# Performance work log

Measured on AMD Instinct MI355X. Metric: run time of the kernel, lower is better.

## Reference

```python
import jax, jax.numpy as jnp
import numpy as np

N_HEAD = 16
HEAD_DIM = 64
WINDOW = 256
ROPE_BASE = 10000.0


def _rope_cos_sin(seq_len, dtype):
    inv_freq = 1.0 / (ROPE_BASE ** (jnp.arange(0, HEAD_DIM, 2, dtype=jnp.float32) / HEAD_DIM))
    t = jnp.arange(seq_len, dtype=jnp.float32)
    freqs = jnp.outer(t, inv_freq)                      # [S, D/2]
    emb = jnp.concatenate([freqs, freqs], axis=-1)      # [S, D]
    return jnp.cos(emb).astype(dtype), jnp.sin(emb).astype(dtype)


def _rotate_half(x):
    x1, x2 = jnp.split(x, 2, axis=-1)
    return jnp.concatenate([-x2, x1], axis=-1)


def _apply_rope(x, cos, sin):
    # x: [B, H, S, D]; cos/sin: [S, D]
    return x * cos[None, None, :, :] + _rotate_half(x) * sin[None, None, :, :]


def setup_inputs() -> dict:
    key = jax.random.key(0)
    ks = jax.random.split(key, 5)
    B, S, E = 2, 2048, 1024
    scale = 1.0 / np.sqrt(E)
    return {
        "x": jax.random.normal(ks[0], (B, S, E), dtype=jnp.float32),
        "Wq": jax.random.normal(ks[1], (E, E), dtype=jnp.float32) * scale,
        "Wk": jax.random.normal(ks[2], (E, E), dtype=jnp.float32) * scale,
        "Wv": jax.random.normal(ks[3], (E, E), dtype=jnp.float32) * scale,
        "Wo": jax.random.normal(ks[4], (E, E), dtype=jnp.float32) * scale,
    }


def reference(x, Wq, Wk, Wv, Wo):
    B, S, E = x.shape
    # QKV projections (nn.Linear: x @ W.T), split heads -> [B, H, S, D]
    def proj(W):
        return (x @ W.T).reshape(B, S, N_HEAD, HEAD_DIM).transpose(0, 2, 1, 3)
    q, k, v = proj(Wq), proj(Wk), proj(Wv)

    cos, sin = _rope_cos_sin(S, x.dtype)
    q = _apply_rope(q, cos, sin)
    k = _apply_rope(k, cos, sin)

    # banded causal mask: attend iff 0 <= i - j < WINDOW
    pos = jnp.arange(S)
    rel = pos[:, None] - pos[None, :]
    allowed = (rel >= 0) & (rel < WINDOW)                # [S, S]

    scale = 1.0 / np.sqrt(HEAD_DIM)
    att = jnp.einsum("bhqd,bhkd->bhqk", q, k) * scale    # [B, H, S, S]
    att = jnp.where(allowed[None, None, :, :], att, -jnp.inf)
    att = jax.nn.softmax(att.astype(jnp.float32), axis=-1).astype(x.dtype)
    y = jnp.einsum("bhqk,bhkd->bhqd", att, v)
    y = y.transpose(0, 2, 1, 3).reshape(B, S, E)
    return y @ Wo.T
```

## Files before the change

kernel.cpp:

```cpp
#include <hip/hip_runtime.h>
#include <cstdint>
#include <cstddef>

#define AS1 __attribute__((address_space(1)))
#define AS3 __attribute__((address_space(3)))

typedef __attribute__((ext_vector_type(4))) float f32x4;
typedef __attribute__((ext_vector_type(2))) float f32x2;
typedef __attribute__((ext_vector_type(8))) short bf16x8;
typedef unsigned short u16;
typedef unsigned int u32;

#define B_ 2
#define S_ 2048
#define E_ 1024
#define H_ 16
#define D_ 64
#define M_ 4096

__device__ __forceinline__ u16 f2bf(float f) {
  union { float f; u32 u; } v; v.f = f;
  u32 u = v.u;
  u32 r = (u + 0x7FFFu + ((u >> 16) & 1u)) >> 16;
  return (u16)r;
}
__device__ __forceinline__ float bf2f(u16 h) {
  union { u32 u; float f; } v; v.u = ((u32)h) << 16;
  return v.f;
}

__device__ __forceinline__ void gl2lds16(const void* g, void* l) {
  __builtin_amdgcn_global_load_lds((const AS1 void*)g, (AS3 void*)l, 16, 0, 0);
}

__global__ __launch_bounds__(256) void prep_kernel(
    const float* __restrict__ x, const float* __restrict__ wq,
    const float* __restrict__ wk, const float* __restrict__ wv,
    const float* __restrict__ wo,
    u16* __restrict__ xb, u16* __restrict__ wqkv, u16* __restrict__ wob,
    float* __restrict__ cstab)
{
  int idx = blockIdx.x * 256 + threadIdx.x;
  const int NX4 = (M_ * E_) / 4;
  const int NW4 = (E_ * E_) / 4;
  const int CONV_TOTAL = NX4 + 4 * NW4;
  if (idx < CONV_TOTAL) {
    const float* src; u16* dst; int off;
    if (idx < NX4)                { src = x;  dst = xb;              off = idx; }
    else if (idx < NX4 + NW4)     { src = wq; dst = wqkv;            off = idx - NX4; }
    else if (idx < NX4 + 2 * NW4) { src = wk; dst = wqkv + E_ * E_;  off = idx - NX4 - NW4; }
    else if (idx < NX4 + 3 * NW4) { src = wv; dst = wqkv + 2 * E_ * E_; off = idx - NX4 - 2 * NW4; }
    else                          { src = wo; dst = wob;             off = idx - NX4 - 3 * NW4; }
    float4 v = reinterpret_cast<const float4*>(src)[off];
    ushort4 o;
    o.x = f2bf(v.x); o.y = f2bf(v.y); o.z = f2bf(v.z); o.w = f2bf(v.w);
    reinterpret_cast<ushort4*>(dst)[off] = o;
  } else if (idx < CONV_TOTAL + S_ * 32) {
    int e = idx - CONV_TOTAL;
    int s = e >> 5, i = e & 31;
    double invf = pow(10000.0, -(double)i / 32.0);
    double ang = (double)s * invf;
    cstab[e * 2]     = (float)cos(ang);
    cstab[e * 2 + 1] = (float)sin(ang);
  }
}

template <int MODE>
__global__ __launch_bounds__(256) void gemm_bt(
    const u16* __restrict__ A, const u16* __restrict__ Bm,
    u16* __restrict__ q_out, u16* __restrict__ k_out, u16* __restrict__ vt_out,
    float* __restrict__ f_out, const float* __restrict__ cstab)
{
  __shared__ __align__(16) u16 smem[17408];
  u16* lA = smem;
  u16* lB = smem + 8192;
  const int tid = threadIdx.x;
  const int w = tid >> 6, l = tid & 63;
  const int lr = l & 15, lg = l >> 4;
  const int mt = blockIdx.y, nt = blockIdx.x;
  const int woffm = (w >> 1) * 64, woffn = (w & 1) * 64;

  const int srow = l >> 3;
  const int scol = ((l & 7) ^ srow) * 8;
  const u16* Abase = A + (size_t)(mt * 128) * 1024;
  const u16* Bbase = Bm + (size_t)(nt * 128) * 1024;

  f32x4 acc[4][4];
#pragma unroll
  for (int i = 0; i < 4; ++i)
#pragma unroll
    for (int j = 0; j < 4; ++j) acc[i][j] = (f32x4){0.f, 0.f, 0.f, 0.f};

  for (int kt = 0; kt < 1024; kt += 64) {
    __syncthreads();
#pragma unroll
    for (int i = 0; i < 4; ++i) {
      int ch = w * 4 + i;
      int row = ch * 8 + srow;
      gl2lds16(Abase + row * 1024 + kt + scol, &lA[ch * 512]);
      gl2lds16(Bbase + row * 1024 + kt + scol, &lB[ch * 512]);
    }
    __syncthreads();
#pragma unroll
    for (int kk = 0; kk < 2; ++kk) {
      bf16x8 av[4], bv[4];
#pragma unroll
      for (int mf = 0; mf < 4; ++mf) {
        int row = woffm + mf * 16 + lr;
        int byteoff = row * 128 + ((kk * 64 + lg * 16) ^ ((row & 7) << 4));
        av[mf] = *(const bf16x8*)((const char*)lA + byteoff);
      }
#pragma unroll
      for (int nf = 0; nf < 4; ++nf) {
        int row = woffn + nf * 16 + lr;
        int byteoff = row * 128 + ((kk * 64 + lg * 16) ^ ((row & 7) << 4));
        bv[nf] = *(const bf16x8*)((const char*)lB + byteoff);
      }
#pragma unroll
      for (int mf = 0; mf < 4; ++mf)
#pragma unroll
        for (int nf = 0; nf < 4; ++nf)
          acc[mf][nf] = __builtin_amdgcn_mfma_f32_16x16x32_bf16(
              av[mf], bv[nf], acc[mf][nf], 0, 0, 0);
    }
  }

  __syncthreads();

  if (MODE == 0) {
    int n0 = nt * 128 + woffn;
    int wsel = n0 >> 10;
    int hh = (n0 >> 6) & 15;
    int stile = mt * 128 + woffm;
    int b = stile >> 11;
    int s0 = stile & 2047;
    if (wsel == 2) {
#pragma unroll
      for (int mf = 0; mf < 4; ++mf) {
        int s = s0 + mf * 16 + lg * 4;
#pragma unroll
        for (int nf = 0; nf < 4; ++nf) {
          int d = nf * 16 + lr;
          ushort4 pk;
          pk.x = f2bf(acc[mf][nf][0]); pk.y = f2bf(acc[mf][nf][1]);
          pk.z = f2bf(acc[mf][nf][2]); pk.w = f2bf(acc[mf][nf][3]);
          *reinterpret_cast<ushort4*>(
              vt_out + ((size_t)(b * 16 + hh) * 64 + d) * 2048 + s) = pk;
        }
      }
    } else {
      u16* lt = smem + w * (64 * 68);
      const f32x2* cst = (const f32x2*)cstab;
#pragma unroll
      for (int mf = 0; mf < 4; ++mf) {
        int sl = mf * 16 + lg * 4;
#pragma unroll
        for (int rr = 0; rr < 4; ++rr) {
          int s = s0 + sl + rr;
#pragma unroll
          for (int nf = 0; nf < 2; ++nf) {
            int i = nf * 16 + lr;
            f32x2 cs = cst[s * 32 + i];
            float a = acc[mf][nf][rr], bb = acc[mf][nf + 2][rr];
            lt[(sl + rr) * 68 + i]      = f2bf(a * cs.x - bb * cs.y);
            lt[(sl + rr) * 68 + 32 + i] = f2bf(bb * cs.x + a * cs.y);
          }
        }
      }
      asm volatile("s_waitcnt lgkmcnt(0)" ::: "memory");
      u16* gout = (wsel == 0 ? q_out : k_out) +
                  ((size_t)(b * 16 + hh) * 2048 + s0) * 64;
      int rl = l >> 3, cc = l & 7;
#pragma unroll
      for (int it = 0; it < 8; ++it) {
        int row = it * 8 + rl;
        bf16x8 v = *(const bf16x8*)(lt + row * 68 + cc * 8);
        *(bf16x8*)(gout + (size_t)row * 64 + cc * 8) = v;
      }
    }
  } else {
#pragma unroll
    for (int mf = 0; mf < 4; ++mf) {
      int m = mt * 128 + woffm + mf * 16 + lg * 4;
#pragma unroll
      for (int nf = 0; nf < 4; ++nf) {
        int n = nt * 128 + woffn + nf * 16 + lr;
#pragma unroll
        for (int rr = 0; rr < 4; ++rr)
          f_out[(size_t)(m + rr) * 1024 + n] = acc[mf][nf][rr];
      }
    }
  }
}

__global__ __launch_bounds__(256) void attn_kernel(
    const u16* __restrict__ qb, const u16* __restrict__ kb,
    const u16* __restrict__ vt, u16* __restrict__ yb)
{
  int blk = blockIdx.x;
  int qt = blk & 31, h = (blk >> 5) & 15, b = blk >> 9;
  int w = threadIdx.x >> 6, l = threadIdx.x & 63;
  int lr = l & 15, lg = l >> 4;
  int qbase = qt * 64 + w * 16;

  const u16* Q  = qb + ((size_t)(b * 16 + h) * 2048) * 64;
  const u16* Kp = kb + ((size_t)(b * 16 + h) * 2048) * 64;
  const u16* Vp = vt + ((size_t)(b * 16 + h) * 64) * 2048;

  __shared__ __align__(16) u16 lds_p[4][16 * 40];
  u16* myp = &lds_p[w][0];

  bf16x8 aq0 = *(const bf16x8*)(Q + (size_t)(qbase + lr) * 64 + lg * 8);
  bf16x8 aq1 = *(const bf16x8*)(Q + (size_t)(qbase + lr) * 64 + 32 + lg * 8);

  f32x4 o[4];
#pragma unroll
  for (int i = 0; i < 4; ++i) o[i] = (f32x4){0.f, 0.f, 0.f, 0.f};
  float mrun[4], lsum[4];
#pragma unroll
  for (int r = 0; r < 4; ++r) { mrun[r] = -1e30f; lsum[r] = 0.f; }

  int kstart = qbase - 255; if (kstart < 0) kstart = 0;
  kstart &= ~31;
  int kend = qbase + 16;
  const float scale = 0.125f;

  for (int kt = kstart; kt < kend; kt += 32) {
    bf16x8 bk0a = *(const bf16x8*)(Kp + (size_t)(kt + lr) * 64 + lg * 8);
    bf16x8 bk0b = *(const bf16x8*)(Kp + (size_t)(kt + lr) * 64 + 32 + lg * 8);
    bf16x8 bk1a = *(const bf16x8*)(Kp + (size_t)(kt + 16 + lr) * 64 + lg * 8);
    bf16x8 bk1b = *(const bf16x8*)(Kp + (size_t)(kt + 16 + lr) * 64 + 32 + lg * 8);
    f32x4 s0 = (f32x4){0.f, 0.f, 0.f, 0.f};
    f32x4 s1 = (f32x4){0.f, 0.f, 0.f, 0.f};
    s0 = __builtin_amdgcn_mfma_f32_16x16x32_bf16(aq0, bk0a, s0, 0, 0, 0);
    s0 = __builtin_amdgcn_mfma_f32_16x16x32_bf16(aq1, bk0b, s0, 0, 0, 0);
    s1 = __builtin_amdgcn_mfma_f32_16x16x32_bf16(aq0, bk1a, s1, 0, 0, 0);
    s1 = __builtin_amdgcn_mfma_f32_16x16x32_bf16(aq1, bk1b, s1, 0, 0, 0);

    float p0[4], p1[4];
#pragma unroll
    for (int r = 0; r < 4; ++r) {
      int q = qbase + lg * 4 + r;
      int k0 = kt + lr, k1 = k0 + 16;
      int r0 = q - k0, r1 = q - k1;
      float v0 = (r0 >= 0 && r0 < 256) ? s0[r] * scale : -1e30f;
      float v1 = (r1 >= 0 && r1 < 256) ? s1[r] * scale : -1e30f;
      float pmax = fmaxf(v0, v1);
      if (!__all(pmax <= mrun[r] + 8.0f)) {
        float mx = pmax;
        mx = fmaxf(mx, __shfl_xor(mx, 1));
        mx = fmaxf(mx, __shfl_xor(mx, 2));
        mx = fmaxf(mx, __shfl_xor(mx, 4));
        mx = fmaxf(mx, __shfl_xor(mx, 8));
        float mnew = fmaxf(mrun[r], mx);
        float f = __expf(mrun[r] - mnew);
        mrun[r] = mnew;
        lsum[r] *= f;
#pragma unroll
        for (int nf = 0; nf < 4; ++nf) o[nf][r] *= f;
      }
      p0[r] = __expf(v0 - mrun[r]);
      p1[r] = __expf(v1 - mrun[r]);
      lsum[r] += p0[r] + p1[r];
    }

#pragma unroll
    for (int r = 0; r < 4; ++r) {
      myp[(lg * 4 + r) * 40 + lr]      = f2bf(p0[r]);
      myp[(lg * 4 + r) * 40 + 16 + lr] = f2bf(p1[r]);
    }
    asm volatile("s_waitcnt lgkmcnt(0)" ::: "memory");
    bf16x8 pa = *(const bf16x8*)((const char*)myp + lr * 80 + lg * 16);
    asm volatile("s_waitcnt lgkmcnt(0)" ::: "memory");

#pragma unroll
    for (int df = 0; df < 4; ++df) {
      bf16x8 vv = *(const bf16x8*)(Vp + (size_t)(df * 16 + lr) * 2048 + kt + lg * 8);
      o[df] = __builtin_amdgcn_mfma_f32_16x16x32_bf16(pa, vv, o[df], 0, 0, 0);
    }
  }

  float lrun[4];
#pragma unroll
  for (int r = 0; r < 4; ++r) {
    float sm = lsum[r];
    sm += __shfl_xor(sm, 1);
    sm += __shfl_xor(sm, 2);
    sm += __shfl_xor(sm, 4);
    sm += __shfl_xor(sm, 8);
    lrun[r] = 1.f / sm;
  }
#pragma unroll
  for (int df = 0; df < 4; ++df)
#pragma unroll
    for (int r = 0; r < 4; ++r) {
      int s = qbase + lg * 4 + r;
      int d = df * 16 + lr;
      yb[((size_t)(b * 2048 + s)) * 1024 + h * 64 + d] = f2bf(o[df][r] * lrun[r]);
    }
}

extern "C" void kernel_launch(void* const* d_in, const int* in_sizes, int n_in,
                              void* d_out, int out_size, void* d_ws, size_t ws_size,
                              hipStream_t stream) {
  const float* x  = (const float*)d_in[0];
  const float* wq = (const float*)d_in[1];
  const float* wk = (const float*)d_in[2];
  const float* wv = (const float*)d_in[3];
  const float* wo = (const float*)d_in[4];

  char* ws = (char*)d_ws;
  const size_t MB = 1u << 20;
  if (ws_size < 49 * MB) return;
  u16*   xb   = (u16*)(ws);
  u16*   wqkv = (u16*)(ws + 8 * MB);
  u16*   wob  = (u16*)(ws + 14 * MB);
  u16*   qb   = (u16*)(ws + 16 * MB);
  u16*   kb   = (u16*)(ws + 24 * MB);
  u16*   vt   = (u16*)(ws + 32 * MB);
  u16*   yb   = (u16*)(ws + 40 * MB);
  float* cst  = (float*)(ws + 48 * MB);
  float* out  = (float*)d_out;

  prep_kernel<<<8448, 256, 0, stream>>>(x, wq, wk, wv, wo, xb, wqkv, wob, cst);
  gemm_bt<0><<<dim3(24, 32), 256, 0, stream>>>(xb, wqkv, qb, kb, vt, nullptr, cst);
  attn_kernel<<<1024, 256, 0, stream>>>(qb, kb, vt, yb);
  gemm_bt<1><<<dim3(8, 32), 256, 0, stream>>>(yb, wob, nullptr, nullptr, nullptr, out, nullptr);
}
```

Before: 190.1 us.

## Rewrite QKV projection GEMM as 256x256 tiled, double-buffered direct-to-LDS pipeline

```diff
diff --git a/kernel.cpp b/kernel.cpp
--- a/kernel.cpp
+++ b/kernel.cpp
@@ -65,13 +65,174 @@
   }
 }
 
-template <int MODE>
-__global__ __launch_bounds__(256) void gemm_bt(
+#define BARR  asm volatile("s_barrier" ::: "memory")
+#define LGKM0 asm volatile("s_waitcnt lgkmcnt(0)" ::: "memory")
+#define VMC6  asm volatile("s_waitcnt vmcnt(6)" ::: "memory")
+#define VMC0  asm volatile("s_waitcnt vmcnt(0)" ::: "memory")
+
+__global__ __launch_bounds__(512, 2) void gemm_qkv(
     const u16* __restrict__ A, const u16* __restrict__ Bm,
     u16* __restrict__ q_out, u16* __restrict__ k_out, u16* __restrict__ vt_out,
-    float* __restrict__ f_out, const float* __restrict__ cstab)
+    const float* __restrict__ cstab)
 {
-  __shared__ __align__(16) u16 smem[17408];
+  __shared__ __align__(16) u16 lds8[65536];
+  const int tid = threadIdx.x;
+  const int w = tid >> 6, l = tid & 63;
+  const int lr = l & 15, lg = l >> 4;
+  const int wm = w >> 2, wn = w & 3;
+
+  int bid = blockIdx.x;
+  int wg = (bid & 7) * 24 + (bid >> 3);
+  int mt = wg / 12, nt = wg % 12;
+
+  const int rA = w * 32 + (l >> 2);
+  const int koff = ((l & 3) ^ ((l >> 3) & 3)) * 8;
+  const u16* aSrc = A + (size_t)(mt * 256 + rA) * 1024 + koff;
+  const u16* bSrc = Bm + (size_t)(nt * 256 + rA) * 1024 + koff;
+  const int aswz = 16 * (lg ^ ((lr >> 1) & 3));
+
+#define STG(isB, ks, bb, t) do { \
+    const u16* s_ = ((isB) ? bSrc : aSrc) + (t) * 64 + (ks) * 32; \
+    u16* d_ = &lds8[(((bb)*2 + (isB))*2 + (ks)) * 8192 + w * 1024]; \
+    gl2lds16(s_, d_); \
+    gl2lds16(s_ + 16 * 1024, d_ + 512); \
+  } while (0)
+
+#define LDA8(qm, ks, bb) do { \
+    const char* sl_ = (const char*)lds8 + (((bb)*2)*2 + (ks)) * 16384; \
+    _Pragma("unroll") for (int mf_ = 0; mf_ < 4; ++mf_) { \
+      int row_ = wm * 128 + (qm) * 64 + mf_ * 16 + lr; \
+      av[mf_] = *(const bf16x8*)(sl_ + row_ * 64 + aswz); \
+    } } while (0)
+
+#define LDB8(ks, bb) do { \
+    const char* sl_ = (const char*)lds8 + (((bb)*2 + 1)*2 + (ks)) * 16384; \
+    _Pragma("unroll") for (int nf_ = 0; nf_ < 4; ++nf_) { \
+      int row_ = wn * 64 + nf_ * 16 + lr; \
+      bv[nf_] = *(const bf16x8*)(sl_ + row_ * 64 + aswz); \
+    } } while (0)
+
+#define MMA16(qm) do { \
+    __builtin_amdgcn_s_setprio(1); \
+    _Pragma("unroll") for (int mf_ = 0; mf_ < 4; ++mf_) \
+    _Pragma("unroll") for (int nf_ = 0; nf_ < 4; ++nf_) \
+      acc[(qm)*4 + mf_][nf_] = __builtin_amdgcn_mfma_f32_16x16x32_bf16( \
+          av[mf_], bv[nf_], acc[(qm)*4 + mf_][nf_], 0, 0, 0); \
+    __builtin_amdgcn_s_setprio(0); \
+  } while (0)
+
+  f32x4 acc[8][4];
+#pragma unroll
+  for (int i = 0; i < 8; ++i)
+#pragma unroll
+    for (int j = 0; j < 4; ++j) acc[i][j] = (f32x4){0.f, 0.f, 0.f, 0.f};
+  bf16x8 av[4], bv[4];
+
+  STG(0, 0, 0, 0); STG(1, 0, 0, 0); STG(0, 1, 0, 0); STG(1, 1, 0, 0);
+  STG(1, 0, 1, 1); STG(0, 0, 1, 1); STG(1, 1, 1, 1);
+  VMC6; BARR;
+
+  for (int i = 0; i < 8; ++i) {
+    LDA8(0, 0, 0); LDB8(0, 0);
+    STG(0, 1, 1, 2 * i + 1);
+    BARR; LGKM0; MMA16(0); BARR;
+    LDA8(1, 0, 0);
+    if (i < 7) STG(1, 0, 0, 2 * i + 2);
+    BARR; LGKM0; MMA16(1); BARR;
+    LDA8(0, 1, 0); LDB8(1, 0);
+    if (i < 7) STG(0, 0, 0, 2 * i + 2);
+    BARR; LGKM0; MMA16(0); BARR;
+    LDA8(1, 1, 0);
+    if (i < 7) STG(1, 1, 0, 2 * i + 2);
+    BARR; LGKM0; MMA16(1);
+    if (i < 7) { VMC6; } else { VMC0; }
+    BARR;
+    LDA8(0, 0, 1); LDB8(0, 1);
+    if (i < 7) STG(0, 1, 0, 2 * i + 2);
+    BARR; LGKM0; MMA16(0); BARR;
+    LDA8(1, 0, 1);
+    if (i < 7) STG(1, 0, 1, 2 * i + 3);
+    BARR; LGKM0; MMA16(1); BARR;
+    LDA8(0, 1, 1); LDB8(1, 1);
+    if (i < 7) STG(0, 0, 1, 2 * i + 3);
+    BARR; LGKM0; MMA16(0); BARR;
+    LDA8(1, 1, 1);
+    if (i < 7) STG(1, 1, 1, 2 * i + 3);
+    BARR; LGKM0; MMA16(1);
+    if (i < 7) VMC6;
+    BARR;
+  }
+  __syncthreads();
+
+  int n0 = nt * 256 + wn * 64;
+  int wsel = n0 >> 10;
+  int hh = (n0 >> 6) & 15;
+  int stile = mt * 256 + wm * 128;
+  int b = stile >> 11;
+  int s0 = stile & 2047;
+
+  if (wsel == 2) {
+#pragma unroll
+    for (int mf = 0; mf < 8; ++mf) {
+      int s = s0 + mf * 16 + lg * 4;
+#pragma unroll
+      for (int nf = 0; nf < 4; ++nf) {
+        int d = nf * 16 + lr;
+        ushort4 pk;
+        pk.x = f2bf(acc[mf][nf][0]); pk.y = f2bf(acc[mf][nf][1]);
+        pk.z = f2bf(acc[mf][nf][2]); pk.w = f2bf(acc[mf][nf][3]);
+        *reinterpret_cast<ushort4*>(
+            vt_out + ((size_t)(b * 16 + hh) * 64 + d) * 2048 + s) = pk;
+      }
+    }
+  } else {
+    u16* gout = (wsel == 0 ? q_out : k_out) +
+                ((size_t)(b * 16 + hh) * 2048 + s0) * 64;
+    u16* lt = &lds8[w * 4352];
+    const f32x2* cst = (const f32x2*)cstab;
+#pragma unroll
+    for (int P = 0; P < 2; ++P) {
+#pragma unroll
+      for (int mf_ = 0; mf_ < 4; ++mf_) {
+        int mf = P * 4 + mf_;
+        int rl = mf_ * 16 + lg * 4;
+#pragma unroll
+        for (int rr = 0; rr < 4; ++rr) {
+          int s = s0 + P * 64 + rl + rr;
+#pragma unroll
+          for (int nf_ = 0; nf_ < 2; ++nf_) {
+            int ii = nf_ * 16 + lr;
+            f32x2 cs = cst[s * 32 + ii];
+            float a = acc[mf][nf_][rr], b2 = acc[mf][nf_ + 2][rr];
+            lt[(rl + rr) * 68 + ii]      = f2bf(a * cs.x - b2 * cs.y);
+            lt[(rl + rr) * 68 + 32 + ii] = f2bf(b2 * cs.x + a * cs.y);
+          }
+        }
+      }
+      LGKM0;
+      {
+        int trl = l >> 3, tcc = l & 7;
+#pragma unroll
+        for (int it = 0; it < 8; ++it) {
+          int row = it * 8 + trl;
+          bf16x8 v = *(const bf16x8*)(lt + row * 68 + tcc * 8);
+          *(bf16x8*)(gout + (size_t)(P * 64 + row) * 64 + tcc * 8) = v;
+        }
+      }
+      LGKM0;
+    }
+  }
+#undef STG
+#undef LDA8
+#undef LDB8
+#undef MMA16
+}
+
+__global__ __launch_bounds__(256) void gemm_out(
+    const u16* __restrict__ A, const u16* __restrict__ Bm,
+    float* __restrict__ f_out)
+{
+  __shared__ __align__(16) u16 smem[16384];
   u16* lA = smem;
   u16* lB = smem + 8192;
   const int tid = threadIdx.x;
@@ -125,70 +286,15 @@
     }
   }
 
-  __syncthreads();
-
-  if (MODE == 0) {
-    int n0 = nt * 128 + woffn;
-    int wsel = n0 >> 10;
-    int hh = (n0 >> 6) & 15;
-    int stile = mt * 128 + woffm;
-    int b = stile >> 11;
-    int s0 = stile & 2047;
-    if (wsel == 2) {
-#pragma unroll
-      for (int mf = 0; mf < 4; ++mf) {
-        int s = s0 + mf * 16 + lg * 4;
-#pragma unroll
-        for (int nf = 0; nf < 4; ++nf) {
-          int d = nf * 16 + lr;
-          ushort4 pk;
-          pk.x = f2bf(acc[mf][nf][0]); pk.y = f2bf(acc[mf][nf][1]);
-          pk.z = f2bf(acc[mf][nf][2]); pk.w = f2bf(acc[mf][nf][3]);
-          *reinterpret_cast<ushort4*>(
-              vt_out + ((size_t)(b * 16 + hh) * 64 + d) * 2048 + s) = pk;
-        }
-      }
-    } else {
-      u16* lt = smem + w * (64 * 68);
-      const f32x2* cst = (const f32x2*)cstab;
-#pragma unroll
-      for (int mf = 0; mf < 4; ++mf) {
-        int sl = mf * 16 + lg * 4;
-#pragma unroll
-        for (int rr = 0; rr < 4; ++rr) {
-          int s = s0 + sl + rr;
-#pragma unroll
-          for (int nf = 0; nf < 2; ++nf) {
-            int i = nf * 16 + lr;
-            f32x2 cs = cst[s * 32 + i];
-            float a = acc[mf][nf][rr], bb = acc[mf][nf + 2][rr];
-            lt[(sl + rr) * 68 + i]      = f2bf(a * cs.x - bb * cs.y);
-            lt[(sl + rr) * 68 + 32 + i] = f2bf(bb * cs.x + a * cs.y);
-          }
-        }
-      }
-      asm volatile("s_waitcnt lgkmcnt(0)" ::: "memory");
-      u16* gout = (wsel == 0 ? q_out : k_out) +
-                  ((size_t)(b * 16 + hh) * 2048 + s0) * 64;
-      int rl = l >> 3, cc = l & 7;
-#pragma unroll
-      for (int it = 0; it < 8; ++it) {
-        int row = it * 8 + rl;
-        bf16x8 v = *(const bf16x8*)(lt + row * 68 + cc * 8);
-        *(bf16x8*)(gout + (size_t)row * 64 + cc * 8) = v;
-      }
-    }
-  } else {
-#pragma unroll
-    for (int mf = 0; mf < 4; ++mf) {
-      int m = mt * 128 + woffm + mf * 16 + lg * 4;
-#pragma unroll
-      for (int nf = 0; nf < 4; ++nf) {
-        int n = nt * 128 + woffn + nf * 16 + lr;
-#pragma unroll
-        for (int rr = 0; rr < 4; ++rr)
-          f_out[(size_t)(m + rr) * 1024 + n] = acc[mf][nf][rr];
-      }
+#pragma unroll
+  for (int mf = 0; mf < 4; ++mf) {
+    int m = mt * 128 + woffm + mf * 16 + lg * 4;
+#pragma unroll
+    for (int nf = 0; nf < 4; ++nf) {
+      int n = nt * 128 + woffn + nf * 16 + lr;
+#pragma unroll
+      for (int rr = 0; rr < 4; ++rr)
+        f_out[(size_t)(m + rr) * 1024 + n] = acc[mf][nf][rr];
     }
   }
 }
@@ -323,7 +429,7 @@
   float* out  = (float*)d_out;
 
   prep_kernel<<<8448, 256, 0, stream>>>(x, wq, wk, wv, wo, xb, wqkv, wob, cst);
-  gemm_bt<0><<<dim3(24, 32), 256, 0, stream>>>(xb, wqkv, qb, kb, vt, nullptr, cst);
+  gemm_qkv<<<192, 512, 0, stream>>>(xb, wqkv, qb, kb, vt, cst);
   attn_kernel<<<1024, 256, 0, stream>>>(qb, kb, vt, yb);
-  gemm_bt<1><<<dim3(8, 32), 256, 0, stream>>>(yb, wob, nullptr, nullptr, nullptr, out, nullptr);
-}
+  gemm_out<<<dim3(8, 32), 256, 0, stream>>>(yb, wob, out);
+}
```

Measured after the change: 179.2 us. 1.06x faster.
